# Kernel tuning notes

Hardware: AMD Instinct MI355X
Metric: run time of the kernel (lower is better)

The kernel has to match this reference:

```python
import jax, jax.numpy as jnp
import numpy as np

TOPK = 12
D = 256
SCALE = D ** -0.5


def setup_inputs() -> dict:
    key = jax.random.key(0)
    ks = jax.random.split(key, 6)
    N, D_in = 12288, 1024
    def w(k, shape, fan_in):
        return jax.random.normal(k, shape, jnp.float32) / np.float32(np.sqrt(fan_in))
    return {
        "x_path": jax.random.normal(ks[0], (N, D_in), jnp.float32),
        "wsi_w": w(ks[1], (D_in, D), D_in),
        "wsi_b": jnp.zeros((D,), jnp.float32),
        "wh_w": w(ks[2], (D, D), D),
        "wh_b": jnp.zeros((D,), jnp.float32),
        "wt_w": w(ks[3], (D, D), D),
        "wt_b": jnp.zeros((D,), jnp.float32),
        "w1_w": w(ks[4], (D, D), D),
        "w1_b": jnp.zeros((D,), jnp.float32),
        "w2_w": w(ks[5], (D, D), D),
        "w2_b": jnp.zeros((D,), jnp.float32),
    }


def reference(x_path, wsi_w, wsi_b, wh_w, wh_b, wt_w, wt_b, w1_w, w1_b, w2_w, w2_b):
    # wsi_net: Linear(1024,256) + ReLU (dropout is identity in eval)
    h = jax.nn.relu(x_path @ wsi_w + wsi_b)          # [N, D]
    e_h = h @ wh_w + wh_b                            # [N, D]
    e_t = h @ wt_w + wt_b                            # [N, D]
    # dense scaled similarity: [N, N]
    attn_logit = (e_h * SCALE) @ e_t.T
    topk_weight, topk_index = jax.lax.top_k(attn_logit, TOPK)  # [N, K]
    topk_prob = jax.nn.softmax(topk_weight, axis=-1)           # [N, K]
    # gather top-k neighbor tail embeddings
    Nb_h = e_t[topk_index]                           # [N, K, D]
    # eh_r = p * Nb_h + (1-p) (x) e_h   (outer product == broadcast mul)
    eh_r = topk_prob[..., None] * Nb_h + (1.0 - topk_prob)[..., None] * e_h[:, None, :]
    gate = jnp.tanh(e_h[:, None, :] + eh_r)          # [N, K, D]
    ka_weight = jnp.einsum('nkd,nkd->nk', Nb_h, gate)  # [N, K]
    ka_prob = jax.nn.softmax(ka_weight, axis=-1)       # [N, K]
    e_Nh = jnp.einsum('nk,nkd->nd', ka_prob, Nb_h)     # [N, D]
    sum_embedding = jax.nn.relu((e_h + e_Nh) @ w1_w + w1_b)
    bi_embedding = jax.nn.relu((e_h * e_Nh) @ w2_w + w2_b)
    return sum_embedding + bi_embedding              # [N, D]
```

## Files before the change

kernel.cpp:

```cpp
#include <hip/hip_runtime.h>
#include <hip/hip_bf16.h>
#include <cmath>

#define TK 12
#define NROW 12288
#define NEG_BIG (-3.0e38f)
#define MFMA16(a,b,c) __builtin_amdgcn_mfma_f32_16x16x32_f16(a,b,c,0,0,0)

#define NCH 8
#define CTILES 96
#define NPH 48
#define NGRP_TOT 384
#define CAP 256

typedef _Float16 f16x8 __attribute__((ext_vector_type(8)));
typedef _Float16 f16x4 __attribute__((ext_vector_type(4)));
typedef float    f32x4 __attribute__((ext_vector_type(4)));

typedef __attribute__((address_space(1))) const void gvoid_t;
typedef __attribute__((address_space(3))) void lvoid_t;
__device__ __forceinline__ void gload_lds16(const void* g, void* l) {
    __builtin_amdgcn_global_load_lds((gvoid_t*)g, (lvoid_t*)l, 16, 0, 0);
}

__global__ __launch_bounds__(256) void wpack(
    const float* __restrict__ W, _Float16* __restrict__ hi,
    _Float16* __restrict__ lo, int N, int nkt)
{
    const int tid = blockIdx.x * 256 + threadIdx.x;
    const int l = tid & 63;
    const int s = (tid >> 6) % nkt;
    const int cg = tid / (nkt * 64);
    const int krow = s * 32 + 8 * (l >> 4);
    const int col = cg * 16 + (l & 15);
    f16x8 H, L;
    #pragma unroll
    for (int j = 0; j < 8; ++j) {
        float w = W[(size_t)(krow + j) * N + col];
        _Float16 h = (_Float16)w;
        H[j] = h;
        L[j] = (_Float16)(w - (float)h);
    }
    *(f16x8*)(hi + (size_t)tid * 8) = H;
    *(f16x8*)(lo + (size_t)tid * 8) = L;
}

__global__ __launch_bounds__(256) void wpack4(
    const float* __restrict__ W0, const float* __restrict__ W1,
    const float* __restrict__ W2, const float* __restrict__ W3,
    _Float16* __restrict__ base)
{
    const int m = blockIdx.y;
    const float* W = (m == 0) ? W0 : (m == 1) ? W1 : (m == 2) ? W2 : W3;
    _Float16* hi = base + (size_t)m * 131072;
    _Float16* lo = hi + 65536;
    const int tid = blockIdx.x * 256 + threadIdx.x;
    const int l = tid & 63;
    const int s = (tid >> 6) & 7;
    const int cg = tid >> 9;
    const int krow = s * 32 + 8 * (l >> 4);
    const int col = cg * 16 + (l & 15);
    f16x8 H, L;
    #pragma unroll
    for (int j = 0; j < 8; ++j) {
        float w = W[(size_t)(krow + j) * 256 + col];
        _Float16 h = (_Float16)w;
        H[j] = h;
        L[j] = (_Float16)(w - (float)h);
    }
    *(f16x8*)(hi + (size_t)tid * 8) = H;
    *(f16x8*)(lo + (size_t)tid * 8) = L;
}

template<bool RELU>
__global__ __launch_bounds__(256) void gemm_mfma(
    const float* __restrict__ A1,
    const _Float16* __restrict__ Wh, const _Float16* __restrict__ Wl,
    const float* __restrict__ bias, float* __restrict__ C, int K)
{
    __shared__ _Float16 aH[2048], aL[2048];
    __shared__ _Float16 wH[2048], wL[2048];
    const int tid = threadIdx.x, lane = tid & 63, wave = tid >> 6;
    const int rb = blockIdx.y * 64;
    const int cbg = blockIdx.x * 4;
    const int nkt = K >> 5;

    const int arow = rb + wave * 16 + (lane & 15);
    const int acol0 = 8 * (lane >> 4);
    const float* a1p = A1 + (size_t)arow * K + acol0;
    const size_t wbase = ((size_t)(cbg + wave) * nkt) * 512 + lane * 8;

    f32x4 acc[4];
    #pragma unroll
    for (int rg = 0; rg < 4; ++rg) acc[rg] = (f32x4){0.f,0.f,0.f,0.f};

    float4 pa0 = *(const float4*)(a1p);
    float4 pa1 = *(const float4*)(a1p + 4);
    f16x8 pwh = *(const f16x8*)(Wh + wbase);
    f16x8 pwl = *(const f16x8*)(Wl + wbase);

    for (int kt = 0; kt < nkt; ++kt) {
        __syncthreads();
        {
            float v[8] = {pa0.x, pa0.y, pa0.z, pa0.w, pa1.x, pa1.y, pa1.z, pa1.w};
            f16x8 H, L;
            #pragma unroll
            for (int j = 0; j < 8; ++j) {
                _Float16 h = (_Float16)v[j];
                H[j] = h;
                L[j] = (_Float16)(v[j] - (float)h);
            }
            *(f16x8*)&aH[tid*8] = H;
            *(f16x8*)&aL[tid*8] = L;
            *(f16x8*)&wH[tid*8] = pwh;
            *(f16x8*)&wL[tid*8] = pwl;
        }
        __syncthreads();
        if (kt + 1 < nkt) {
            pa0 = *(const float4*)(a1p + (kt+1)*32);
            pa1 = *(const float4*)(a1p + (kt+1)*32 + 4);
            pwh = *(const f16x8*)(Wh + wbase + (size_t)(kt+1)*512);
            pwl = *(const f16x8*)(Wl + wbase + (size_t)(kt+1)*512);
        }
        f16x8 wh = *(const f16x8*)&wH[(wave*64 + lane)*8];
        f16x8 wl = *(const f16x8*)&wL[(wave*64 + lane)*8];
        #pragma unroll
        for (int rg = 0; rg < 4; ++rg) {
            f16x8 ah = *(const f16x8*)&aH[(rg*64 + lane)*8];
            f16x8 al = *(const f16x8*)&aL[(rg*64 + lane)*8];
            acc[rg] = MFMA16(wh, ah, acc[rg]);
            acc[rg] = MFMA16(wl, ah, acc[rg]);
            acc[rg] = MFMA16(wh, al, acc[rg]);
        }
    }
    const int col = (cbg + wave)*16 + 4*(lane >> 4);
    float4 b4 = *(const float4*)(bias + col);
    #pragma unroll
    for (int rg = 0; rg < 4; ++rg) {
        const int row = rb + rg*16 + (lane & 15);
        float4 o;
        o.x = acc[rg][0] + b4.x; o.y = acc[rg][1] + b4.y;
        o.z = acc[rg][2] + b4.z; o.w = acc[rg][3] + b4.w;
        if (RELU) {
            o.x = fmaxf(o.x, 0.f); o.y = fmaxf(o.y, 0.f);
            o.z = fmaxf(o.z, 0.f); o.w = fmaxf(o.w, 0.f);
        }
        *(float4*)(C + (size_t)row*256 + col) = o;
    }
}

template<int DMODE>
__global__ __launch_bounds__(256) void gemm_dual(
    const float* __restrict__ A1, const float* __restrict__ A2,
    const _Float16* __restrict__ W1h, const _Float16* __restrict__ W1l,
    const _Float16* __restrict__ W2h, const _Float16* __restrict__ W2l,
    const float* __restrict__ bias1, const float* __restrict__ bias2,
    float* __restrict__ C1, float* __restrict__ C2,
    _Float16* __restrict__ P1, _Float16* __restrict__ P2)
{
    __shared__ _Float16 aH[2][2048], aL[2][2048];
    __shared__ _Float16 wH[2][2048], wL[2][2048];
    const int tid = threadIdx.x, lane = tid & 63, wave = tid >> 6;
    const int rb = blockIdx.y * 64;
    const int cbg = blockIdx.x * 4;

    const int arow = rb + wave * 16 + (lane & 15);
    const int acol0 = 8 * (lane >> 4);
    const float* a1p = A1 + (size_t)arow * 256 + acol0;
    const float* a2p = (DMODE == 1) ? (A2 + (size_t)arow * 256 + acol0) : nullptr;
    const size_t wbase = ((size_t)(cbg + wave) * 8) * 512 + lane * 8;

    f32x4 acc1[4], acc2[4];
    #pragma unroll
    for (int rg = 0; rg < 4; ++rg) {
        acc1[rg] = (f32x4){0.f,0.f,0.f,0.f};
        acc2[rg] = (f32x4){0.f,0.f,0.f,0.f};
    }

    float4 pa0 = *(const float4*)(a1p);
    float4 pa1 = *(const float4*)(a1p + 4);
    float4 pb0, pb1;
    if (DMODE == 1) { pb0 = *(const float4*)(a2p); pb1 = *(const float4*)(a2p + 4); }
    f16x8 pw1h = *(const f16x8*)(W1h + wbase);
    f16x8 pw1l = *(const f16x8*)(W1l + wbase);
    f16x8 pw2h = *(const f16x8*)(W2h + wbase);
    f16x8 pw2l = *(const f16x8*)(W2l + wbase);

    for (int kt = 0; kt < 8; ++kt) {
        __syncthreads();
        {
            float v[8] = {pa0.x, pa0.y, pa0.z, pa0.w, pa1.x, pa1.y, pa1.z, pa1.w};
            if (DMODE == 0) {
                f16x8 H, L;
                #pragma unroll
                for (int j = 0; j < 8; ++j) {
                    _Float16 h = (_Float16)v[j];
                    H[j] = h;
                    L[j] = (_Float16)(v[j] - (float)h);
                }
                *(f16x8*)&aH[0][tid*8] = H;
                *(f16x8*)&aL[0][tid*8] = L;
            } else {
                float b[8] = {pb0.x, pb0.y, pb0.z, pb0.w, pb1.x, pb1.y, pb1.z, pb1.w};
                f16x8 Hs, Ls, Hm, Lm;
                #pragma unroll
                for (int j = 0; j < 8; ++j) {
                    float s = v[j] + b[j];
                    float m = v[j] * b[j];
                    _Float16 hs = (_Float16)s;
                    _Float16 hm = (_Float16)m;
                    Hs[j] = hs; Ls[j] = (_Float16)(s - (float)hs);
                    Hm[j] = hm; Lm[j] = (_Float16)(m - (float)hm);
                }
                *(f16x8*)&aH[0][tid*8] = Hs;
                *(f16x8*)&aL[0][tid*8] = Ls;
                *(f16x8*)&aH[1][tid*8] = Hm;
                *(f16x8*)&aL[1][tid*8] = Lm;
            }
            *(f16x8*)&wH[0][tid*8] = pw1h;
            *(f16x8*)&wL[0][tid*8] = pw1l;
            *(f16x8*)&wH[1][tid*8] = pw2h;
            *(f16x8*)&wL[1][tid*8] = pw2l;
        }
        __syncthreads();
        if (kt + 1 < 8) {
            pa0 = *(const float4*)(a1p + (kt+1)*32);
            pa1 = *(const float4*)(a1p + (kt+1)*32 + 4);
            if (DMODE == 1) {
                pb0 = *(const float4*)(a2p + (kt+1)*32);
                pb1 = *(const float4*)(a2p + (kt+1)*32 + 4);
            }
            pw1h = *(const f16x8*)(W1h + wbase + (size_t)(kt+1)*512);
            pw1l = *(const f16x8*)(W1l + wbase + (size_t)(kt+1)*512);
            pw2h = *(const f16x8*)(W2h + wbase + (size_t)(kt+1)*512);
            pw2l = *(const f16x8*)(W2l + wbase + (size_t)(kt+1)*512);
        }
        f16x8 w1h = *(const f16x8*)&wH[0][(wave*64 + lane)*8];
        f16x8 w1l = *(const f16x8*)&wL[0][(wave*64 + lane)*8];
        f16x8 w2h = *(const f16x8*)&wH[1][(wave*64 + lane)*8];
        f16x8 w2l = *(const f16x8*)&wL[1][(wave*64 + lane)*8];
        #pragma unroll
        for (int rg = 0; rg < 4; ++rg) {
            f16x8 ah0 = *(const f16x8*)&aH[0][(rg*64 + lane)*8];
            f16x8 al0 = *(const f16x8*)&aL[0][(rg*64 + lane)*8];
            acc1[rg] = MFMA16(w1h, ah0, acc1[rg]);
            acc1[rg] = MFMA16(w1l, ah0, acc1[rg]);
            acc1[rg] = MFMA16(w1h, al0, acc1[rg]);
            f16x8 ah1 = (DMODE == 1) ? *(const f16x8*)&aH[1][(rg*64 + lane)*8] : ah0;
            f16x8 al1 = (DMODE == 1) ? *(const f16x8*)&aL[1][(rg*64 + lane)*8] : al0;
            acc2[rg] = MFMA16(w2h, ah1, acc2[rg]);
            acc2[rg] = MFMA16(w2l, ah1, acc2[rg]);
            acc2[rg] = MFMA16(w2h, al1, acc2[rg]);
        }
    }
    const int col = (cbg + wave)*16 + 4*(lane >> 4);
    float4 b14 = *(const float4*)(bias1 + col);
    float4 b24 = *(const float4*)(bias2 + col);
    #pragma unroll
    for (int rg = 0; rg < 4; ++rg) {
        const int row = rb + rg*16 + (lane & 15);
        if (DMODE == 0) {
            float4 o1, o2;
            o1.x = acc1[rg][0] + b14.x; o1.y = acc1[rg][1] + b14.y;
            o1.z = acc1[rg][2] + b14.z; o1.w = acc1[rg][3] + b14.w;
            o2.x = acc2[rg][0] + b24.x; o2.y = acc2[rg][1] + b24.y;
            o2.z = acc2[rg][2] + b24.z; o2.w = acc2[rg][3] + b24.w;
            *(float4*)(C1 + (size_t)row*256 + col) = o1;
            *(float4*)(C2 + (size_t)row*256 + col) = o2;
            const size_t poff = ((size_t)(row >> 4)*8 + (col >> 5))*512
                              + (((col & 31) >> 3)*16 + (row & 15))*8 + (col & 7);
            f16x4 p1, p2;
            p1[0] = (_Float16)(o1.x * 0.0625f); p1[1] = (_Float16)(o1.y * 0.0625f);
            p1[2] = (_Float16)(o1.z * 0.0625f); p1[3] = (_Float16)(o1.w * 0.0625f);
            p2[0] = (_Float16)o2.x; p2[1] = (_Float16)o2.y;
            p2[2] = (_Float16)o2.z; p2[3] = (_Float16)o2.w;
            *(f16x4*)(P1 + poff) = p1;
            *(f16x4*)(P2 + poff) = p2;
        } else {
            float4 o;
            o.x = fmaxf(acc1[rg][0] + b14.x, 0.f) + fmaxf(acc2[rg][0] + b24.x, 0.f);
            o.y = fmaxf(acc1[rg][1] + b14.y, 0.f) + fmaxf(acc2[rg][1] + b24.y, 0.f);
            o.z = fmaxf(acc1[rg][2] + b14.z, 0.f) + fmaxf(acc2[rg][2] + b24.z, 0.f);
            o.w = fmaxf(acc1[rg][3] + b14.w, 0.f) + fmaxf(acc2[rg][3] + b24.w, 0.f);
            *(float4*)(C1 + (size_t)row*256 + col) = o;
        }
    }
}

__global__ __launch_bounds__(256, 2) void s1_gmax(
    const _Float16* __restrict__ ehh, const _Float16* __restrict__ eth,
    unsigned* __restrict__ g32, unsigned char* __restrict__ gcol)
{
    __shared__ _Float16 abuf[3][8192];
    const int tid = threadIdx.x, lane = tid & 63, wave = tid >> 6;
    const int chunk = blockIdx.x & (NCH-1);
    const int rblk = blockIdx.x >> 3;
    const int rg0 = rblk * 8 + wave * 2;

    f16x8 bh[2][8];
    #pragma unroll
    for (int rs = 0; rs < 2; ++rs) {
        const _Float16* p = ehh + (size_t)(rg0 + rs)*4096 + lane*8;
        #pragma unroll
        for (int s = 0; s < 8; ++s) bh[rs][s] = *(const f16x8*)(p + s*512);
    }
    #pragma unroll
    for (int rs = 0; rs < 2; ++rs)
        #pragma unroll
        for (int s = 0; s < 8; ++s)
            asm volatile("" : "+v"(bh[rs][s]));

    const int rsw = (lane >> 4) & 1;
    const int myrow = (rg0 + rsw)*16 + (lane & 15);
    const size_t rowbase = (size_t)myrow*NGRP_TOT + chunk*NPH;

    const _Float16* gsrc = eth + (size_t)chunk * CTILES * 4096;
    #pragma unroll
    for (int ph = 0; ph < 2; ++ph) {
        #pragma unroll
        for (int i = 0; i < 4; ++i) {
            const int u = wave*4 + i;
            gload_lds16(gsrc + (size_t)(ph*2 + (u>>3))*4096 + (u&7)*512 + lane*8,
                        &abuf[ph][u*512]);
        }
    }
    asm volatile("s_waitcnt vmcnt(4) lgkmcnt(0)" ::: "memory");
    __builtin_amdgcn_s_barrier();
    asm volatile("" ::: "memory");

    int cur = 0;
    for (int pp = 0; pp < 6; ++pp) {
        unsigned resv[8];
        unsigned long long colv = 0;
        #pragma unroll
        for (int q = 0; q < 8; ++q) {
            const int p = pp*8 + q;
            int nx = cur + 2; if (nx >= 3) nx -= 3;
            if (p + 2 < NPH) {
                #pragma unroll
                for (int i = 0; i < 4; ++i) {
                    const int u = wave*4 + i;
                    gload_lds16(gsrc + (size_t)((p+2)*2 + (u>>3))*4096 + (u&7)*512 + lane*8,
                                &abuf[nx][u*512]);
                }
            }
            float m1a = NEG_BIG, m2a = NEG_BIG; int mca = 0;
            float m1b = NEG_BIG, m2b = NEG_BIG; int mcb = 0;
            #pragma unroll
            for (int tt = 0; tt < 2; ++tt) {
                f32x4 aE[2], aO[2];
                #pragma unroll
                for (int rs = 0; rs < 2; ++rs) {
                    aE[rs] = (f32x4){0.f,0.f,0.f,0.f};
                    aO[rs] = (f32x4){0.f,0.f,0.f,0.f};
                }
                #pragma unroll
                for (int s = 0; s < 8; ++s) {
                    f16x8 ah = *(const f16x8*)&abuf[cur][tt*4096 + s*512 + lane*8];
                    if (s & 1) {
                        aO[0] = MFMA16(ah, bh[0][s], aO[0]);
                        aO[1] = MFMA16(ah, bh[1][s], aO[1]);
                    } else {
                        aE[0] = MFMA16(ah, bh[0][s], aE[0]);
                        aE[1] = MFMA16(ah, bh[1][s], aE[1]);
                    }
                }
                f32x4 a0 = aE[0] + aO[0];
                f32x4 a1 = aE[1] + aO[1];
                const int cb = tt*16 + 4*(lane >> 4);
                #pragma unroll
                for (int e = 0; e < 4; ++e) {
                    bool g0 = a0[e] > m1a;
                    m2a = fmaxf(m2a, g0 ? m1a : a0[e]);
                    mca = g0 ? (cb + e) : mca;
                    m1a = fmaxf(m1a, a0[e]);
                    bool g1 = a1[e] > m1b;
                    m2b = fmaxf(m2b, g1 ? m1b : a1[e]);
                    mcb = g1 ? (cb + e) : mcb;
                    m1b = fmaxf(m1b, a1[e]);
                }
            }
            #pragma unroll
            for (int k = 16; k <= 32; k <<= 1) {
                float o1 = __shfl_xor(m1a, k); int oc = __shfl_xor(mca, k);
                float o2 = __shfl_xor(m2a, k);
                bool gt = o1 > m1a;
                m2a = fmaxf(fmaxf(m2a, o2), gt ? m1a : o1);
                mca = gt ? oc : mca;
                m1a = fmaxf(m1a, o1);
                float p1 = __shfl_xor(m1b, k); int pc = __shfl_xor(mcb, k);
                float p2 = __shfl_xor(m2b, k);
                bool ht = p1 > m1b;
                m2b = fmaxf(fmaxf(m2b, p2), ht ? m1b : p1);
                mcb = ht ? pc : mcb;
                m1b = fmaxf(m1b, p1);
            }
            {
                float M1 = rsw ? m1b : m1a;
                float M2 = rsw ? m2b : m2a;
                int   MC = rsw ? mcb : mca;
                unsigned short h1 = __builtin_bit_cast(unsigned short, (_Float16)M1);
                unsigned short h2 = __builtin_bit_cast(unsigned short, (_Float16)M2);
                resv[q] = ((unsigned)h1 << 16) | h2;
                colv |= (unsigned long long)(unsigned char)MC << (8*q);
            }
            if (q == 7 && lane < 32) {
                const size_t base = rowbase + pp*8;
                uint4 v0; v0.x = resv[0]; v0.y = resv[1]; v0.z = resv[2]; v0.w = resv[3];
                uint4 v1; v1.x = resv[4]; v1.y = resv[5]; v1.z = resv[6]; v1.w = resv[7];
                *(uint4*)(g32 + base)     = v0;
                *(uint4*)(g32 + base + 4) = v1;
                *(unsigned long long*)(gcol + base) = colv;
            }
            if (p + 2 < NPH) {
                if (q == 7) { asm volatile("s_waitcnt vmcnt(7)" ::: "memory"); }
                else        { asm volatile("s_waitcnt vmcnt(4)" ::: "memory"); }
            } else {
                asm volatile("s_waitcnt vmcnt(0)" ::: "memory");
            }
            __builtin_amdgcn_s_barrier();
            asm volatile("" ::: "memory");
            cur = cur + 1; if (cur >= 3) cur = 0;
        }
    }
    asm volatile("s_waitcnt vmcnt(0)" ::: "memory");
}

__global__ __launch_bounds__(256) void b2_emit(
    const unsigned* __restrict__ g32, const unsigned char* __restrict__ gcol,
    unsigned* __restrict__ cnt, int* __restrict__ cand)
{
    const int lane = threadIdx.x & 63;
    const int wave = threadIdx.x >> 6;
    const int row  = blockIdx.x * 4 + wave;

    const unsigned* gr = g32 + (size_t)row*NGRP_TOT + lane*6;
    uint2 u0 = *(const uint2*)gr;
    uint2 u1 = *(const uint2*)(gr + 2);
    uint2 u2 = *(const uint2*)(gr + 4);
    unsigned uu[6] = {u0.x, u0.y, u1.x, u1.y, u2.x, u2.y};
    float m1[6], m2[6];
    #pragma unroll
    for (int i = 0; i < 6; ++i) {
        m1[i] = (float)__builtin_bit_cast(_Float16, (unsigned short)(uu[i] >> 16));
        m2[i] = (float)__builtin_bit_cast(_Float16, (unsigned short)(uu[i] & 0xffffu));
    }

    float sl[6];
    #pragma unroll
    for (int j = 0; j < 6; ++j) sl[j] = NEG_BIG;
    #pragma unroll
    for (int i = 0; i < 6; ++i) {
        float v = m1[i];
        #pragma unroll
        for (int j = 5; j >= 1; --j)
            sl[j] = __builtin_amdgcn_fmed3f(v, sl[j], sl[j-1]);
        sl[0] = fmaxf(v, sl[0]);
    }

    int hi = 0;
    float t12 = NEG_BIG;
    #pragma unroll 1
    for (int o = 0; o < TK; ++o) {
        float head = (hi < 6) ? sl[hi] : NEG_BIG;
        float bv = head; int bl = lane;
        #pragma unroll
        for (int off = 1; off <= 32; off <<= 1) {
            float ov = __shfl_xor(bv, off);
            int   ol = __shfl_xor(bl, off);
            bool take = (ov > bv) || (ov == bv && ol < bl);
            bv = take ? ov : bv;
            bl = take ? ol : bl;
        }
        if (lane == bl) hi++;
        t12 = bv;
    }
    const float tau = t12 - 0.02f;

    int n = 0;
    int* crow = cand + (size_t)row * CAP;
    #pragma unroll 1
    for (int i = 0; i < 6; ++i) {
        const bool hit1 = m1[i] >= tau;
        const bool expn = hit1 && (m2[i] >= tau);
        const bool single = hit1 && !expn;
        unsigned long long ms = __ballot(single);
        if (single) {
            const int pos = n + __popcll(ms & ((1ull << lane) - 1ull));
            if (pos < CAP) {
                const int g = lane*6 + i;
                crow[pos] = g*32 + (int)gcol[(size_t)row*NGRP_TOT + g];
            }
        }
        n += __popcll(ms);
        unsigned long long me = __ballot(expn);
        while (me) {
            const int src = __builtin_ctzll(me);
            me &= me - 1ull;
            const int cb = (src*6 + i) * 32;
            if (lane < 32) {
                const int pos = n + lane;
                if (pos < CAP) crow[pos] = cb + lane;
            }
            n += 32;
        }
    }
    if (lane == 0) cnt[row] = (unsigned)((n < CAP) ? n : CAP);
}

__global__ __launch_bounds__(256) void s3_tail(
    const float* __restrict__ e_h, const float* __restrict__ e_t,
    const unsigned int* __restrict__ cnt, const int* __restrict__ cand,
    float* __restrict__ e_Nh)
{
    const int lane = threadIdx.x & 63;
    const int wave = threadIdx.x >> 6;
    const int row  = blockIdx.x * 4 + wave;

    const unsigned cn = min(cnt[row], (unsigned)CAP);
    const float* ehr = e_h + (size_t)row * 256;

    float v[4]; int c[4];
    #pragma unroll
    for (int i = 0; i < 4; ++i) {
        const int idx = lane + 64*i;
        const bool act = idx < (int)cn;
        c[i] = act ? cand[(size_t)row*CAP + idx] : (0x7ffffff0 + i);
        v[i] = NEG_BIG;
        if ((int)cn > 64*i) {
            const float* etr = e_t + (size_t)(act ? c[i] : 0) * 256;
            float s = 0.f;
            for (int k = 0; k < 64; ++k) {
                float4 a = *(const float4*)(ehr + k*4);
                float4 b = *(const float4*)(etr + k*4);
                s += a.x*b.x + a.y*b.y + a.z*b.z + a.w*b.w;
            }
            if (act) v[i] = s * 0.0625f;
        }
    }

    float tvv[TK]; int ti[TK];
    #pragma unroll
    for (int o = 0; o < TK; ++o) {
        float bv = v[0]; int bc = c[0];
        #pragma unroll
        for (int i = 1; i < 4; ++i) {
            bool take = (v[i] > bv) || (v[i] == bv && c[i] < bc);
            bv = take ? v[i] : bv;
            bc = take ? c[i] : bc;
        }
        #pragma unroll
        for (int off = 32; off; off >>= 1) {
            float ov = __shfl_xor(bv, off);
            int   oc = __shfl_xor(bc, off);
            bool take = (ov > bv) || (ov == bv && oc < bc);
            bv = take ? ov : bv;
            bc = take ? oc : bc;
        }
        tvv[o] = bv; ti[o] = bc;
        #pragma unroll
        for (int i = 0; i < 4; ++i)
            if (c[i] == bc) v[i] = NEG_BIG;
    }

    float p[TK]; float Z = 0.f;
    #pragma unroll
    for (int j = 0; j < TK; ++j) { p[j] = expf(tvv[j] - tvv[0]); Z += p[j]; }
    const float invZ = 1.f / Z;
    #pragma unroll
    for (int j = 0; j < TK; ++j) p[j] *= invZ;

    float4 eh = *(const float4*)(ehr + lane * 4);

    float4 nb[TK]; float kw[TK];
    #pragma unroll
    for (int k = 0; k < TK; ++k) {
        float4 n = *(const float4*)(e_t + (size_t)ti[k] * 256 + lane * 4);
        nb[k] = n;
        const float pk = p[k], qk = 1.f - p[k];
        float4 gt;
        gt.x = tanhf(eh.x + (pk * n.x + qk * eh.x));
        gt.y = tanhf(eh.y + (pk * n.y + qk * eh.y));
        gt.z = tanhf(eh.z + (pk * n.z + qk * eh.z));
        gt.w = tanhf(eh.w + (pk * n.w + qk * eh.w));
        float d = n.x*gt.x + n.y*gt.y + n.z*gt.z + n.w*gt.w;
        #pragma unroll
        for (int off = 32; off; off >>= 1) d += __shfl_xor(d, off);
        kw[k] = d;
    }

    float km = kw[0];
    #pragma unroll
    for (int k = 1; k < TK; ++k) km = fmaxf(km, kw[k]);
    float kz = 0.f; float kp[TK];
    #pragma unroll
    for (int k = 0; k < TK; ++k) { kp[k] = expf(kw[k] - km); kz += kp[k]; }
    const float invKZ = 1.f / kz;

    float4 acc = make_float4(0.f, 0.f, 0.f, 0.f);
    #pragma unroll
    for (int k = 0; k < TK; ++k) {
        acc.x += kp[k] * nb[k].x;
        acc.y += kp[k] * nb[k].y;
        acc.z += kp[k] * nb[k].z;
        acc.w += kp[k] * nb[k].w;
    }
    acc.x *= invKZ; acc.y *= invKZ; acc.z *= invKZ; acc.w *= invKZ;
    *(float4*)(e_Nh + (size_t)row * 256 + lane * 4) = acc;
}

extern "C" void kernel_launch(void* const* d_in, const int* in_sizes, int n_in,
                              void* d_out, int out_size, void* d_ws, size_t ws_size,
                              hipStream_t stream)
{
    (void)in_sizes; (void)n_in; (void)out_size; (void)ws_size;
    const float* x     = (const float*)d_in[0];
    const float* wsi_w = (const float*)d_in[1];
    const float* wsi_b = (const float*)d_in[2];
    const float* wh_w  = (const float*)d_in[3];
    const float* wh_b  = (const float*)d_in[4];
    const float* wt_w  = (const float*)d_in[5];
    const float* wt_b  = (const float*)d_in[6];
    const float* w1_w  = (const float*)d_in[7];
    const float* w1_b  = (const float*)d_in[8];
    const float* w2_w  = (const float*)d_in[9];
    const float* w2_b  = (const float*)d_in[10];
    float* out = (float*)d_out;
    float* ws  = (float*)d_ws;

    const int M = NROW;
    const size_t ND = (size_t)M * 256;

    float* h    = ws;
    float* e_h  = ws + ND;
    float* e_t  = ws + 2*ND;
    _Float16* ehh = (_Float16*)(ws + 3*ND);
    _Float16* eth = (_Float16*)(ws + 3*ND + ND/2);
    size_t o = 4*ND;
    unsigned* g32 = (unsigned*)(ws + o);          o += (size_t)NGRP_TOT*NROW;
    unsigned char* gcol = (unsigned char*)(ws + o); o += (size_t)NGRP_TOT*NROW/4;
    unsigned int* cnt = (unsigned int*)(ws + o);  o += NROW;
    int* cand = (int*)(ws + o);                   o += (size_t)NROW*CAP;
    _Float16* hp = (_Float16*)(ws + o);
    _Float16* wsiH = hp;
    _Float16* wsiL = hp + 262144;
    _Float16* w4base = hp + 524288;
    _Float16* whH  = w4base;
    _Float16* whL  = w4base + 65536;
    _Float16* wtH  = w4base + 2*65536;
    _Float16* wtL  = w4base + 3*65536;
    _Float16* w1H  = w4base + 4*65536;
    _Float16* w1L  = w4base + 5*65536;
    _Float16* w2H  = w4base + 6*65536;
    _Float16* w2L  = w4base + 7*65536;
    float* e_Nh = h;

    wpack<<<128, 256, 0, stream>>>(wsi_w, wsiH, wsiL, 256, 32);
    wpack4<<<dim3(32, 4), 256, 0, stream>>>(wh_w, wt_w, w1_w, w2_w, w4base);

    gemm_mfma<true><<<dim3(4, M/64), 256, 0, stream>>>(
        x, wsiH, wsiL, wsi_b, h, 1024);
    gemm_dual<0><<<dim3(4, M/64), 256, 0, stream>>>(
        h, nullptr, whH, whL, wtH, wtL, wh_b, wt_b, e_h, e_t, ehh, eth);
    s1_gmax<<<NCH*96, 256, 0, stream>>>(ehh, eth, g32, gcol);
    b2_emit<<<M/4, 256, 0, stream>>>(g32, gcol, cnt, cand);
    s3_tail<<<M/4, 256, 0, stream>>>(e_h, e_t, cnt, cand, e_Nh);
    gemm_dual<1><<<dim3(4, M/64), 256, 0, stream>>>(
        e_h, e_Nh, w1H, w1L, w2H, w2L, w1_b, w2_b, out, nullptr, nullptr, nullptr);
}
```

Before: 313.4 us.

## Widen similarity kernel to four row groups per wave over sixteen column chunks

Each wave in the top-k pre-pass now holds four 16-row query groups in registers instead of two. Each LDS-staged key tile therefore feeds twice as many MFMAs. The column range is split into 16 chunks of 48 tiles instead of 8 of 96, which keeps the block count the same and halves the loop length. It also raises wave priority around the MFMA block; the gain in operand reuse costs more registers per thread, which may cut occupancy.

```diff
diff --git a/kernel.cpp b/kernel.cpp
--- a/kernel.cpp
+++ b/kernel.cpp
@@ -7,9 +7,9 @@
 #define NEG_BIG (-3.0e38f)
 #define MFMA16(a,b,c) __builtin_amdgcn_mfma_f32_16x16x32_f16(a,b,c,0,0,0)
 
-#define NCH 8
-#define CTILES 96
-#define NPH 48
+#define NCH16 16
+#define CT16 48
+#define NPH16 24
 #define NGRP_TOT 384
 #define CAP 256
 
@@ -293,28 +293,28 @@
 {
     __shared__ _Float16 abuf[3][8192];
     const int tid = threadIdx.x, lane = tid & 63, wave = tid >> 6;
-    const int chunk = blockIdx.x & (NCH-1);
-    const int rblk = blockIdx.x >> 3;
-    const int rg0 = rblk * 8 + wave * 2;
-
-    f16x8 bh[2][8];
-    #pragma unroll
-    for (int rs = 0; rs < 2; ++rs) {
+    const int chunk = blockIdx.x & (NCH16-1);
+    const int rblk = blockIdx.x >> 4;
+    const int rg0 = rblk * 16 + wave * 4;
+
+    f16x8 bh[4][8];
+    #pragma unroll
+    for (int rs = 0; rs < 4; ++rs) {
         const _Float16* p = ehh + (size_t)(rg0 + rs)*4096 + lane*8;
         #pragma unroll
         for (int s = 0; s < 8; ++s) bh[rs][s] = *(const f16x8*)(p + s*512);
     }
     #pragma unroll
-    for (int rs = 0; rs < 2; ++rs)
+    for (int rs = 0; rs < 4; ++rs)
         #pragma unroll
         for (int s = 0; s < 8; ++s)
             asm volatile("" : "+v"(bh[rs][s]));
 
-    const int rsw = (lane >> 4) & 1;
+    const int rsw = lane >> 4;
     const int myrow = (rg0 + rsw)*16 + (lane & 15);
-    const size_t rowbase = (size_t)myrow*NGRP_TOT + chunk*NPH;
-
-    const _Float16* gsrc = eth + (size_t)chunk * CTILES * 4096;
+    const size_t rowbase = (size_t)myrow*NGRP_TOT + chunk*NPH16;
+
+    const _Float16* gsrc = eth + (size_t)chunk * CT16 * 4096;
     #pragma unroll
     for (int ph = 0; ph < 2; ++ph) {
         #pragma unroll
@@ -329,14 +329,14 @@
     asm volatile("" ::: "memory");
 
     int cur = 0;
-    for (int pp = 0; pp < 6; ++pp) {
+    for (int pp = 0; pp < 3; ++pp) {
         unsigned resv[8];
         unsigned long long colv = 0;
         #pragma unroll
         for (int q = 0; q < 8; ++q) {
             const int p = pp*8 + q;
             int nx = cur + 2; if (nx >= 3) nx -= 3;
-            if (p + 2 < NPH) {
+            if (p + 2 < NPH16) {
                 #pragma unroll
                 for (int i = 0; i < 4; ++i) {
                     const int u = wave*4 + i;
@@ -344,67 +344,65 @@
                                 &abuf[nx][u*512]);
                 }
             }
-            float m1a = NEG_BIG, m2a = NEG_BIG; int mca = 0;
-            float m1b = NEG_BIG, m2b = NEG_BIG; int mcb = 0;
+            float m1[4], m2[4]; int mc[4];
+            #pragma unroll
+            for (int r = 0; r < 4; ++r) { m1[r] = NEG_BIG; m2[r] = NEG_BIG; mc[r] = 0; }
+            __builtin_amdgcn_s_setprio(1);
             #pragma unroll
             for (int tt = 0; tt < 2; ++tt) {
-                f32x4 aE[2], aO[2];
+                f32x4 aE[4], aO[4];
                 #pragma unroll
-                for (int rs = 0; rs < 2; ++rs) {
-                    aE[rs] = (f32x4){0.f,0.f,0.f,0.f};
-                    aO[rs] = (f32x4){0.f,0.f,0.f,0.f};
+                for (int r = 0; r < 4; ++r) {
+                    aE[r] = (f32x4){0.f,0.f,0.f,0.f};
+                    aO[r] = (f32x4){0.f,0.f,0.f,0.f};
                 }
                 #pragma unroll
                 for (int s = 0; s < 8; ++s) {
                     f16x8 ah = *(const f16x8*)&abuf[cur][tt*4096 + s*512 + lane*8];
                     if (s & 1) {
-                        aO[0] = MFMA16(ah, bh[0][s], aO[0]);
-                        aO[1] = MFMA16(ah, bh[1][s], aO[1]);
+                        #pragma unroll
+                        for (int r = 0; r < 4; ++r) aO[r] = MFMA16(ah, bh[r][s], aO[r]);
                     } else {
-                        aE[0] = MFMA16(ah, bh[0][s], aE[0]);
-                        aE[1] = MFMA16(ah, bh[1][s], aE[1]);
+                        #pragma unroll
+                        for (int r = 0; r < 4; ++r) aE[r] = MFMA16(ah, bh[r][s], aE[r]);
                     }
                 }
-                f32x4 a0 = aE[0] + aO[0];
-                f32x4 a1 = aE[1] + aO[1];
                 const int cb = tt*16 + 4*(lane >> 4);
                 #pragma unroll
-                for (int e = 0; e < 4; ++e) {
-                    bool g0 = a0[e] > m1a;
-                    m2a = fmaxf(m2a, g0 ? m1a : a0[e]);
-                    mca = g0 ? (cb + e) : mca;
-                    m1a = fmaxf(m1a, a0[e]);
-                    bool g1 = a1[e] > m1b;
-                    m2b = fmaxf(m2b, g1 ? m1b : a1[e]);
-                    mcb = g1 ? (cb + e) : mcb;
-                    m1b = fmaxf(m1b, a1[e]);
+                for (int r = 0; r < 4; ++r) {
+                    f32x4 a = aE[r] + aO[r];
+                    #pragma unroll
+                    for (int e = 0; e < 4; ++e) {
+                        bool g0 = a[e] > m1[r];
+                        m2[r] = fmaxf(m2[r], g0 ? m1[r] : a[e]);
+                        mc[r] = g0 ? (cb + e) : mc[r];
+                        m1[r] = fmaxf(m1[r], a[e]);
+                    }
                 }
             }
+            __builtin_amdgcn_s_setprio(0);
             #pragma unroll
-            for (int k = 16; k <= 32; k <<= 1) {
-                float o1 = __shfl_xor(m1a, k); int oc = __shfl_xor(mca, k);
-                float o2 = __shfl_xor(m2a, k);
-                bool gt = o1 > m1a;
-                m2a = fmaxf(fmaxf(m2a, o2), gt ? m1a : o1);
-                mca = gt ? oc : mca;
-                m1a = fmaxf(m1a, o1);
-                float p1 = __shfl_xor(m1b, k); int pc = __shfl_xor(mcb, k);
-                float p2 = __shfl_xor(m2b, k);
-                bool ht = p1 > m1b;
-                m2b = fmaxf(fmaxf(m2b, p2), ht ? m1b : p1);
-                mcb = ht ? pc : mcb;
-                m1b = fmaxf(m1b, p1);
+            for (int r = 0; r < 4; ++r) {
+                #pragma unroll
+                for (int k = 16; k <= 32; k <<= 1) {
+                    float o1 = __shfl_xor(m1[r], k); int oc = __shfl_xor(mc[r], k);
+                    float o2 = __shfl_xor(m2[r], k);
+                    bool gt = o1 > m1[r];
+                    m2[r] = fmaxf(fmaxf(m2[r], o2), gt ? m1[r] : o1);
+                    mc[r] = gt ? oc : mc[r];
+                    m1[r] = fmaxf(m1[r], o1);
+                }
             }
             {
-                float M1 = rsw ? m1b : m1a;
-                float M2 = rsw ? m2b : m2a;
-                int   MC = rsw ? mcb : mca;
+                float M1 = (rsw == 0) ? m1[0] : (rsw == 1) ? m1[1] : (rsw == 2) ? m1[2] : m1[3];
+                float M2 = (rsw == 0) ? m2[0] : (rsw == 1) ? m2[1] : (rsw == 2) ? m2[2] : m2[3];
+                int   MC = (rsw == 0) ? mc[0] : (rsw == 1) ? mc[1] : (rsw == 2) ? mc[2] : mc[3];
                 unsigned short h1 = __builtin_bit_cast(unsigned short, (_Float16)M1);
                 unsigned short h2 = __builtin_bit_cast(unsigned short, (_Float16)M2);
                 resv[q] = ((unsigned)h1 << 16) | h2;
                 colv |= (unsigned long long)(unsigned char)MC << (8*q);
             }
-            if (q == 7 && lane < 32) {
+            if (q == 7) {
                 const size_t base = rowbase + pp*8;
                 uint4 v0; v0.x = resv[0]; v0.y = resv[1]; v0.z = resv[2]; v0.w = resv[3];
                 uint4 v1; v1.x = resv[4]; v1.y = resv[5]; v1.z = resv[6]; v1.w = resv[7];
@@ -412,7 +410,7 @@
                 *(uint4*)(g32 + base + 4) = v1;
                 *(unsigned long long*)(gcol + base) = colv;
             }
-            if (p + 2 < NPH) {
+            if (p + 2 < NPH16) {
                 if (q == 7) { asm volatile("s_waitcnt vmcnt(7)" ::: "memory"); }
                 else        { asm volatile("s_waitcnt vmcnt(4)" ::: "memory"); }
             } else {
@@ -662,7 +660,7 @@
         x, wsiH, wsiL, wsi_b, h, 1024);
     gemm_dual<0><<<dim3(4, M/64), 256, 0, stream>>>(
         h, nullptr, whH, whL, wtH, wtL, wh_b, wt_b, e_h, e_t, ehh, eth);
-    s1_gmax<<<NCH*96, 256, 0, stream>>>(ehh, eth, g32, gcol);
+    s1_gmax<<<NCH16*48, 256, 0, stream>>>(ehh, eth, g32, gcol);
     b2_emit<<<M/4, 256, 0, stream>>>(g32, gcol, cnt, cand);
     s3_tail<<<M/4, 256, 0, stream>>>(e_h, e_t, cnt, cand, e_Nh);
     gemm_dual<1><<<dim3(4, M/64), 256, 0, stream>>>(
```

Result: slower. 369.1 us (+17.8%).

## Coalesce candidate rescoring loads and raise wave priority around MFMA block

Applied to the files above, without the earlier changes.

The tail kernel's exact rescoring of candidate columns is reorganized. Previously each lane read a whole 1 KB e_t row alone. Now four lanes share one candidate, each reading interleaved float4 chunks, with the e_h row held in registers. Partial sums are reduced by shuffles and staged through shared memory. This gives more coalesced gathers, at the cost of extra shuffles, LDS traffic and register pressure. Separately, s_setprio is raised around the MFMA and top-2 section of the similarity kernel to favour issuing compute over other waves.

```diff
diff --git a/kernel.cpp b/kernel.cpp
--- a/kernel.cpp
+++ b/kernel.cpp
@@ -346,6 +346,7 @@
             }
             float m1a = NEG_BIG, m2a = NEG_BIG; int mca = 0;
             float m1b = NEG_BIG, m2b = NEG_BIG; int mcb = 0;
+            __builtin_amdgcn_s_setprio(1);
             #pragma unroll
             for (int tt = 0; tt < 2; ++tt) {
                 f32x4 aE[2], aO[2];
@@ -380,6 +381,7 @@
                     m1b = fmaxf(m1b, a1[e]);
                 }
             }
+            __builtin_amdgcn_s_setprio(0);
             #pragma unroll
             for (int k = 16; k <= 32; k <<= 1) {
                 float o1 = __shfl_xor(m1a, k); int oc = __shfl_xor(mca, k);
@@ -513,30 +515,51 @@
     const unsigned int* __restrict__ cnt, const int* __restrict__ cand,
     float* __restrict__ e_Nh)
 {
+    __shared__ float sbuf[4][64];
     const int lane = threadIdx.x & 63;
     const int wave = threadIdx.x >> 6;
     const int row  = blockIdx.x * 4 + wave;
-
-    const unsigned cn = min(cnt[row], (unsigned)CAP);
+    const int quad = lane & 3;
+    const int cg   = lane >> 2;
+
+    const int cn = (int)min(cnt[row], (unsigned)CAP);
     const float* ehr = e_h + (size_t)row * 256;
+
+    float4 ehv[16];
+    #pragma unroll
+    for (int j = 0; j < 16; ++j)
+        ehv[j] = *(const float4*)(ehr + j*16 + quad*4);
 
     float v[4]; int c[4];
     #pragma unroll
     for (int i = 0; i < 4; ++i) {
         const int idx = lane + 64*i;
-        const bool act = idx < (int)cn;
-        c[i] = act ? cand[(size_t)row*CAP + idx] : (0x7ffffff0 + i);
+        c[i] = (idx < cn) ? cand[(size_t)row*CAP + idx] : (0x7ffffff0 + i);
         v[i] = NEG_BIG;
-        if ((int)cn > 64*i) {
-            const float* etr = e_t + (size_t)(act ? c[i] : 0) * 256;
+    }
+
+    #pragma unroll 1
+    for (int ch = 0; ch < 4; ++ch) {
+        if (cn <= 64*ch) break;
+        #pragma unroll
+        for (int b = 0; b < 4; ++b) {
+            const int ci = ch*64 + b*16 + cg;
+            const bool act = ci < cn;
+            const int col = act ? cand[(size_t)row*CAP + ci] : 0;
+            const float* etr = e_t + (size_t)col * 256;
             float s = 0.f;
-            for (int k = 0; k < 64; ++k) {
-                float4 a = *(const float4*)(ehr + k*4);
-                float4 b = *(const float4*)(etr + k*4);
-                s += a.x*b.x + a.y*b.y + a.z*b.z + a.w*b.w;
-            }
-            if (act) v[i] = s * 0.0625f;
-        }
+            #pragma unroll
+            for (int j = 0; j < 16; ++j) {
+                float4 bb = *(const float4*)(etr + j*16 + quad*4);
+                s += ehv[j].x*bb.x + ehv[j].y*bb.y + ehv[j].z*bb.z + ehv[j].w*bb.w;
+            }
+            s += __shfl_xor(s, 1);
+            s += __shfl_xor(s, 2);
+            if (quad == 0) sbuf[wave][b*16 + cg] = s;
+        }
+        const int idx = ch*64 + lane;
+        float sv = sbuf[wave][lane];
+        if (idx < cn) v[ch] = sv * 0.0625f;
     }
 
     float tvv[TK]; int ti[TK];
```

Measured after the change: 343.8 us. +9.7%, slower.
